# Optimization experiments

Hardware: AMD Instinct MI355X
Metric: run time of the kernel (lower is better)

## Reference

```python
import jax, jax.numpy as jnp
import numpy as np

NUM_HEADS = 16
D_MODEL = 1024
BATCH = 4
SEQ = 1024


def setup_inputs() -> dict:
    key = jax.random.key(0)
    k_x, k_m, k_wqkv, k_bqkv, k_wo, k_bo = jax.random.split(key, 6)
    d = D_MODEL
    scale = 1.0 / np.sqrt(d)
    return {
        "x": jax.random.normal(k_x, (BATCH, SEQ, d), dtype=jnp.float32),
        "mask": jax.random.randint(k_m, (BATCH, SEQ, SEQ), 0, 2, dtype=jnp.int32),
        "Wqkv": jax.random.normal(k_wqkv, (d, 3 * d), dtype=jnp.float32) * scale,
        "bqkv": jax.random.normal(k_bqkv, (3 * d,), dtype=jnp.float32) * 0.02,
        "Wo": jax.random.normal(k_wo, (d, d), dtype=jnp.float32) * scale,
        "bo": jax.random.normal(k_bo, (d,), dtype=jnp.float32) * 0.02,
    }


def reference(x, mask, Wqkv, bqkv, Wo, bo):
    B, S, D = x.shape
    H = NUM_HEADS
    hd = D // H
    # fused QKV projection: [B,S,3D] -> [B,S,H,3*hd] -> [B,H,S,3*hd]
    qkv = (x @ Wqkv + bqkv).reshape(B, S, H, 3 * hd).transpose(0, 2, 1, 3)
    q, k, v = jnp.split(qkv, 3, axis=-1)  # each [B,H,S,hd]
    # scores [B,H,S,S], scaled by sqrt(head_dim)
    scores = jnp.einsum("bhqd,bhkd->bhqk", q, k) / jnp.sqrt(jnp.float32(hd))
    scores = jnp.where(mask[:, None, :, :] == 0, jnp.float32(-1e20), scores)
    attn = jax.nn.softmax(scores, axis=-1)
    vals = jnp.einsum("bhqk,bhkd->bhqd", attn, v)  # [B,H,S,hd]
    vals = vals.transpose(0, 2, 1, 3).reshape(B, S, D)
    return vals @ Wo + bo
```

## Files before the change

### kernel.cpp

```cpp
#include <hip/hip_runtime.h>
#include <cstddef>
#include <cstdint>

#define BATCH 4
#define SEQ   1024
#define DM    1024
#define NH    16
#define HD    64
#define D3    3072
#define LOG2E 1.44269504088896340736f
#define QSCALE (0.125f * LOG2E)

typedef _Float16 f16x8 __attribute__((ext_vector_type(8)));
typedef _Float16 f16x4 __attribute__((ext_vector_type(4)));
typedef __fp16   h16x2 __attribute__((ext_vector_type(2)));
typedef float    f32x4 __attribute__((ext_vector_type(4)));

#define MFMA16(a, b, c) __builtin_amdgcn_mfma_f32_16x16x32_f16((a), (b), (c), 0, 0, 0)
#define GLD_LDS16(gp, lp) \
  __builtin_amdgcn_global_load_lds((const __attribute__((address_space(1))) unsigned int*)(gp), \
                                   (__attribute__((address_space(3))) unsigned int*)(lp), 16, 0, 0)
#if __has_builtin(__builtin_amdgcn_exp2f)
#define EXP2(x) __builtin_amdgcn_exp2f(x)
#else
#define EXP2(x) exp2f(x)
#endif

__global__ __launch_bounds__(256) void prep_all(const float* __restrict__ x,
                                                _Float16* __restrict__ x16,
                                                const int* __restrict__ mask,
                                                unsigned long long* __restrict__ mb,
                                                const float* __restrict__ W1,
                                                _Float16* __restrict__ WT1,
                                                const float* __restrict__ W2,
                                                _Float16* __restrict__ WT2) {
  __shared__ _Float16 T[64 * 72];
  const int tid = threadIdx.x;
  const int bx = blockIdx.x;
  if (bx < 1024) {
    const int tx = bx & 63, ty = bx >> 6;
    const bool first = tx < 48;
    const float* W = first ? W1 : W2;
    _Float16* WT = first ? WT1 : WT2;
    const int N = first ? D3 : DM;
    const int K = DM;
    const int c0 = (first ? tx : (tx - 48)) * 64;
    const int r0 = ty * 64;
#pragma unroll
    for (int it = 0; it < 4; ++it) {
      const int row = it * 16 + (tid >> 4);
      const int col4 = (tid & 15) * 4;
      float4 wv = *(const float4*)(W + (size_t)(r0 + row) * N + c0 + col4);
      T[(col4 + 0) * 72 + row] = (_Float16)wv.x;
      T[(col4 + 1) * 72 + row] = (_Float16)wv.y;
      T[(col4 + 2) * 72 + row] = (_Float16)wv.z;
      T[(col4 + 3) * 72 + row] = (_Float16)wv.w;
    }
    __syncthreads();
#pragma unroll
    for (int it = 0; it < 2; ++it) {
      const int g = it * 256 + tid;
      const int col = g >> 3, seg = g & 7;
      *(f16x8*)(WT + (size_t)(c0 + col) * K + r0 + seg * 8) =
          *(const f16x8*)(T + col * 72 + seg * 8);
    }
  } else if (bx < 3072) {
    const int i = (bx - 1024) * 256 + tid;
    float4 a = ((const float4*)x)[i * 2];
    float4 b = ((const float4*)x)[i * 2 + 1];
    f16x8 o;
    o[0] = (_Float16)a.x; o[1] = (_Float16)a.y; o[2] = (_Float16)a.z; o[3] = (_Float16)a.w;
    o[4] = (_Float16)b.x; o[5] = (_Float16)b.y; o[6] = (_Float16)b.z; o[7] = (_Float16)b.w;
    ((f16x8*)x16)[i] = o;
  } else {
    const size_t i = (size_t)(bx - 3072) * 256 + tid;
    const int m = mask[i];
    unsigned long long bits = __ballot(m != 0);
    if ((tid & 63) == 0) mb[i >> 6] = bits;
  }
}

template <typename OutT, bool QKV, int TN, int BK>
__global__ __launch_bounds__(256) void gemm_bt(const _Float16* __restrict__ A,
                                               const _Float16* __restrict__ BT,
                                               const float* __restrict__ bias,
                                               OutT* __restrict__ C,
                                               _Float16* __restrict__ vTp,
                                               int M, int N, int K) {
  constexpr int NT = TN / 32;
  constexpr int CH = BK / 8;
  __shared__ _Float16 As[128 * BK];
  __shared__ _Float16 Bs[TN * BK];
  const int tid = threadIdx.x;
  const int l15 = tid & 15;
  const int quad = (tid & 63) >> 4;
  const int w = tid >> 6;
  const int wm = w >> 1, wn = w & 1;
  const int rowbase = blockIdx.y * 128;
  const int colbase = blockIdx.x * TN;

  f32x4 acc[4][NT];
#pragma unroll
  for (int mt = 0; mt < 4; ++mt)
#pragma unroll
    for (int nt = 0; nt < NT; ++nt) acc[mt][nt] = (f32x4){0.f, 0.f, 0.f, 0.f};

  for (int k0 = 0; k0 < K; k0 += BK) {
    __syncthreads();
#pragma unroll
    for (int it = 0; it < 128 * CH / 256; ++it) {
      const int g = it * 256 + tid;
      const int r = g / CH, cs = (g & (CH - 1)) ^ (r & (CH - 1));
      GLD_LDS16(A + (size_t)(rowbase + r) * K + k0 + cs * 8, As + g * 8);
    }
#pragma unroll
    for (int it = 0; it < TN * CH / 256; ++it) {
      const int g = it * 256 + tid;
      const int r = g / CH, cs = (g & (CH - 1)) ^ (r & (CH - 1));
      GLD_LDS16(BT + (size_t)(colbase + r) * K + k0 + cs * 8, Bs + g * 8);
    }
    __syncthreads();
#pragma unroll
    for (int kh = 0; kh < BK / 32; ++kh) {
      f16x8 a[4], b[NT];
#pragma unroll
      for (int mt = 0; mt < 4; ++mt) {
        const int row = wm * 64 + mt * 16 + l15;
        a[mt] = *(const f16x8*)(As + row * BK +
                                (((kh * 4 + quad) ^ (row & (CH - 1))) << 3));
      }
#pragma unroll
      for (int nt = 0; nt < NT; ++nt) {
        const int row = wn * (TN / 2) + nt * 16 + l15;
        b[nt] = *(const f16x8*)(Bs + row * BK +
                                (((kh * 4 + quad) ^ (row & (CH - 1))) << 3));
      }
#pragma unroll
      for (int mt = 0; mt < 4; ++mt)
#pragma unroll
        for (int nt = 0; nt < NT; ++nt)
          acc[mt][nt] = MFMA16(a[mt], b[nt], acc[mt][nt]);
    }
  }

  float bv[NT];
#pragma unroll
  for (int nt = 0; nt < NT; ++nt) bv[nt] = bias[colbase + wn * (TN / 2) + nt * 16 + l15];
#pragma unroll
  for (int mt = 0; mt < 4; ++mt)
#pragma unroll
    for (int nt = 0; nt < NT; ++nt) {
      const int col = colbase + wn * (TN / 2) + nt * 16 + l15;
      if (QKV) {
        const int reg3 = (col >> 6) % 3;
        if (reg3 == 2) {
          const int hh = col / 192;
          const int d = col - hh * 192 - 128;
          const int row0 = rowbase + wm * 64 + mt * 16 + quad * 4;
          const int bb = row0 >> 10, s0 = row0 & 1023;
          f16x4 pk;
#pragma unroll
          for (int r = 0; r < 4; ++r) pk[r] = (_Float16)(acc[mt][nt][r] + bv[nt]);
          *(f16x4*)(vTp + ((size_t)((bb * NH + hh) * HD + d)) * SEQ + s0) = pk;
        } else {
          const float sc = (reg3 == 0) ? QSCALE : 1.f;
#pragma unroll
          for (int r = 0; r < 4; ++r) {
            const int row = rowbase + wm * 64 + mt * 16 + quad * 4 + r;
            C[(size_t)row * N + col] = (OutT)((acc[mt][nt][r] + bv[nt]) * sc);
          }
        }
      } else {
#pragma unroll
        for (int r = 0; r < 4; ++r) {
          const int row = rowbase + wm * 64 + mt * 16 + quad * 4 + r;
          C[(size_t)row * N + col] = (OutT)(acc[mt][nt][r] + bv[nt]);
        }
      }
    }
}

__global__ __launch_bounds__(256) void attn(const _Float16* __restrict__ qkv,
                                            const _Float16* __restrict__ vT,
                                            const unsigned long long* __restrict__ mb,
                                            _Float16* __restrict__ vals) {
  __shared__ _Float16 Ks[64 * 72];
  __shared__ _Float16 Vt[64 * 72];
  __shared__ _Float16 Ps[4][32 * 72];
  __shared__ __align__(8) _Float16 LUT[16][4];
  const int tid = threadIdx.x;
  const int l15 = tid & 15, quad = (tid & 63) >> 4, w = tid >> 6;
  const int i = blockIdx.x;
  const int bh = (i >> 6) * 8 + (i & 7);
  const int b = bh >> 4, h = bh & 15;
  const int q0 = ((i >> 3) & 7) << 7;

  if (tid < 16) {
    LUT[tid][0] = (tid & 1) ? (_Float16)1.f : (_Float16)0.f;
    LUT[tid][1] = (tid & 2) ? (_Float16)1.f : (_Float16)0.f;
    LUT[tid][2] = (tid & 4) ? (_Float16)1.f : (_Float16)0.f;
    LUT[tid][3] = (tid & 8) ? (_Float16)1.f : (_Float16)0.f;
  }

  const _Float16* qb = qkv + (size_t)b * SEQ * D3 + h * 192;
  f16x8 qf[2][2];
#pragma unroll
  for (int qn = 0; qn < 2; ++qn)
#pragma unroll
    for (int hf = 0; hf < 2; ++hf)
      qf[qn][hf] = *(const f16x8*)(qb + (size_t)(q0 + w * 32 + qn * 16 + l15) * D3 +
                                   hf * 32 + quad * 8);

  const _Float16* kg = qb + 64;
  const _Float16* vg = vT + (size_t)((b * NH + h) * HD) * SEQ;
  const int sr = tid >> 3, sseg = tid & 7;
  const int vd = tid >> 2, vs = tid & 3;
  const size_t mb0 = (size_t)(b * SEQ + q0 + w * 32 + l15) * 16;
  const size_t mb1 = (size_t)(b * SEQ + q0 + w * 32 + 16 + l15) * 16;

  f16x8 k0r = *(const f16x8*)(kg + (size_t)sr * D3 + sseg * 8);
  f16x8 k1r = *(const f16x8*)(kg + (size_t)(sr + 32) * D3 + sseg * 8);
  f16x8 v0r = *(const f16x8*)(vg + (size_t)vd * SEQ + vs * 8);
  f16x8 v1r = *(const f16x8*)(vg + (size_t)vd * SEQ + 32 + vs * 8);
  unsigned long long mr0 = mb[mb0], mr1 = mb[mb1];

  f32x4 lacc[2];
  f32x4 o_[2][4];
#pragma unroll
  for (int qn = 0; qn < 2; ++qn) {
    lacc[qn] = (f32x4){0.f, 0.f, 0.f, 0.f};
#pragma unroll
    for (int dt = 0; dt < 4; ++dt) o_[qn][dt] = (f32x4){0.f, 0.f, 0.f, 0.f};
  }
  f16x8 ones;
#pragma unroll
  for (int i2 = 0; i2 < 8; ++i2) ones[i2] = (_Float16)1.f;

  for (int kt = 0; kt < 16; ++kt) {
    if (kt) __syncthreads();
    *(f16x8*)(Ks + sr * 72 + sseg * 8) = k0r;
    *(f16x8*)(Ks + (sr + 32) * 72 + sseg * 8) = k1r;
    *(f16x8*)(Vt + vd * 72 + vs * 8) = v0r;
    *(f16x8*)(Vt + vd * 72 + 32 + vs * 8) = v1r;
    __syncthreads();
    const unsigned long long mc[2] = {mr0, mr1};
    if (kt < 15) {
      const int kn = (kt + 1) << 6;
      k0r = *(const f16x8*)(kg + (size_t)(kn + sr) * D3 + sseg * 8);
      k1r = *(const f16x8*)(kg + (size_t)(kn + sr + 32) * D3 + sseg * 8);
      v0r = *(const f16x8*)(vg + (size_t)vd * SEQ + kn + vs * 8);
      v1r = *(const f16x8*)(vg + (size_t)vd * SEQ + kn + 32 + vs * 8);
      mr0 = mb[mb0 + kt + 1];
      mr1 = mb[mb1 + kt + 1];
    }
    f32x4 st[4][2];
#pragma unroll
    for (int mt = 0; mt < 4; ++mt)
#pragma unroll
      for (int qn = 0; qn < 2; ++qn) st[mt][qn] = (f32x4){0.f, 0.f, 0.f, 0.f};
#pragma unroll
    for (int mt = 0; mt < 4; ++mt) {
      f16x8 ka0 = *(const f16x8*)(Ks + (mt * 16 + l15) * 72 + quad * 8);
      f16x8 ka1 = *(const f16x8*)(Ks + (mt * 16 + l15) * 72 + 32 + quad * 8);
#pragma unroll
      for (int qn = 0; qn < 2; ++qn) {
        st[mt][qn] = MFMA16(ka0, qf[qn][0], st[mt][qn]);
        st[mt][qn] = MFMA16(ka1, qf[qn][1], st[mt][qn]);
      }
    }
#pragma unroll
    for (int qn = 0; qn < 2; ++qn)
#pragma unroll
      for (int mt = 0; mt < 4; ++mt) {
        float e0 = EXP2(fminf(st[mt][qn][0], 15.f));
        float e1 = EXP2(fminf(st[mt][qn][1], 15.f));
        float e2 = EXP2(fminf(st[mt][qn][2], 15.f));
        float e3 = EXP2(fminf(st[mt][qn][3], 15.f));
        h16x2 lo = __builtin_amdgcn_cvt_pkrtz(e0, e1);
        h16x2 hi = __builtin_amdgcn_cvt_pkrtz(e2, e3);
        f16x4 pk;
        pk[0] = (_Float16)lo[0]; pk[1] = (_Float16)lo[1];
        pk[2] = (_Float16)hi[0]; pk[3] = (_Float16)hi[1];
        const unsigned nib = (unsigned)(mc[qn] >> (mt * 16 + quad * 4)) & 15u;
        pk *= *(const f16x4*)LUT[nib];
        *(f16x4*)(&Ps[w][(qn * 16 + l15) * 72 + mt * 16 + quad * 4]) = pk;
      }
    f16x8 pa[2][2];
#pragma unroll
    for (int qn = 0; qn < 2; ++qn) {
      pa[qn][0] = *(const f16x8*)(&Ps[w][(qn * 16 + l15) * 72 + quad * 8]);
      pa[qn][1] = *(const f16x8*)(&Ps[w][(qn * 16 + l15) * 72 + 32 + quad * 8]);
      lacc[qn] = MFMA16(pa[qn][0], ones, lacc[qn]);
      lacc[qn] = MFMA16(pa[qn][1], ones, lacc[qn]);
    }
#pragma unroll
    for (int dt = 0; dt < 4; ++dt) {
      f16x8 vb0 = *(const f16x8*)(Vt + (dt * 16 + l15) * 72 + quad * 8);
      f16x8 vb1 = *(const f16x8*)(Vt + (dt * 16 + l15) * 72 + 32 + quad * 8);
#pragma unroll
      for (int qn = 0; qn < 2; ++qn) {
        o_[qn][dt] = MFMA16(pa[qn][0], vb0, o_[qn][dt]);
        o_[qn][dt] = MFMA16(pa[qn][1], vb1, o_[qn][dt]);
      }
    }
  }
#pragma unroll
  for (int qn = 0; qn < 2; ++qn) {
    f32x4 inv;
#pragma unroll
    for (int r = 0; r < 4; ++r) inv[r] = 1.f / lacc[qn][r];
#pragma unroll
    for (int dt = 0; dt < 4; ++dt)
#pragma unroll
      for (int r = 0; r < 4; ++r)
        vals[(size_t)(b * SEQ + q0 + w * 32 + qn * 16 + quad * 4 + r) * DM +
             h * HD + dt * 16 + l15] = (_Float16)(o_[qn][dt][r] * inv[r]);
  }
}

extern "C" void kernel_launch(void* const* d_in, const int* in_sizes, int n_in,
                              void* d_out, int out_size, void* d_ws, size_t ws_size,
                              hipStream_t stream) {
  const float* x    = (const float*)d_in[0];
  const int*   mask = (const int*)  d_in[1];
  const float* Wqkv = (const float*)d_in[2];
  const float* bqkv = (const float*)d_in[3];
  const float* Wo   = (const float*)d_in[4];
  const float* bo   = (const float*)d_in[5];
  float* out = (float*)d_out;

  char* ws = (char*)d_ws;
  _Float16* qkv16  = (_Float16*)ws;                    ws += (size_t)BATCH*SEQ*D3*2;
  _Float16* vT16   = (_Float16*)ws;                    ws += (size_t)BATCH*DM*SEQ*2;
  _Float16* x16    = (_Float16*)ws;                    ws += (size_t)BATCH*SEQ*DM*2;
  _Float16* WqkvT  = (_Float16*)ws;                    ws += (size_t)DM*D3*2;
  _Float16* WoT    = (_Float16*)ws;                    ws += (size_t)DM*DM*2;
  _Float16* vals16 = (_Float16*)ws;                    ws += (size_t)BATCH*SEQ*DM*2;
  unsigned long long* mbits = (unsigned long long*)ws;

  prep_all<<<3072 + (BATCH*SEQ*SEQ)/256, 256, 0, stream>>>(
      x, x16, mask, mbits, Wqkv, WqkvT, Wo, WoT);

  gemm_bt<_Float16, true, 128, 64><<<dim3(D3/128, BATCH*SEQ/128), 256, 0, stream>>>(
      x16, WqkvT, bqkv, qkv16, vT16, BATCH*SEQ, D3, DM);
  attn<<<512, 256, 0, stream>>>(qkv16, vT16, mbits, vals16);
  gemm_bt<float, false, 64, 128><<<dim3(DM/64, (BATCH*SEQ)/128), 256, 0, stream>>>(
      vals16, WoT, bo, out, nullptr, BATCH*SEQ, DM, DM);
}
```

Before: 186.1 us.

## Double-buffer K/V tiles in attention and raise wave priority around MFMA

The attention kernel now keeps two LDS buffers for K and V. While the current tile is being computed, the next tile is written into the other buffer and global loads are issued two tiles ahead, which cuts the per-iteration barriers from two to one. s_setprio is also raised around the MFMA blocks so matrix work is favoured when waves contend. In exchange, K/V LDS use doubles and more registers stay live for the deeper prefetch, which may lower occupancy.

```diff
diff --git a/kernel.cpp b/kernel.cpp
--- a/kernel.cpp
+++ b/kernel.cpp
@@ -184,8 +184,8 @@
                                             const _Float16* __restrict__ vT,
                                             const unsigned long long* __restrict__ mb,
                                             _Float16* __restrict__ vals) {
-  __shared__ _Float16 Ks[64 * 72];
-  __shared__ _Float16 Vt[64 * 72];
+  __shared__ _Float16 Ks[2][64 * 72];
+  __shared__ _Float16 Vt[2][64 * 72];
   __shared__ _Float16 Ps[4][32 * 72];
   __shared__ __align__(8) _Float16 LUT[16][4];
   const int tid = threadIdx.x;
@@ -222,7 +222,16 @@
   f16x8 k1r = *(const f16x8*)(kg + (size_t)(sr + 32) * D3 + sseg * 8);
   f16x8 v0r = *(const f16x8*)(vg + (size_t)vd * SEQ + vs * 8);
   f16x8 v1r = *(const f16x8*)(vg + (size_t)vd * SEQ + 32 + vs * 8);
-  unsigned long long mr0 = mb[mb0], mr1 = mb[mb1];
+  unsigned long long mcur0 = mb[mb0], mcur1 = mb[mb1];
+  *(f16x8*)(Ks[0] + sr * 72 + sseg * 8) = k0r;
+  *(f16x8*)(Ks[0] + (sr + 32) * 72 + sseg * 8) = k1r;
+  *(f16x8*)(Vt[0] + vd * 72 + vs * 8) = v0r;
+  *(f16x8*)(Vt[0] + vd * 72 + 32 + vs * 8) = v1r;
+  k0r = *(const f16x8*)(kg + (size_t)(64 + sr) * D3 + sseg * 8);
+  k1r = *(const f16x8*)(kg + (size_t)(64 + sr + 32) * D3 + sseg * 8);
+  v0r = *(const f16x8*)(vg + (size_t)vd * SEQ + 64 + vs * 8);
+  v1r = *(const f16x8*)(vg + (size_t)vd * SEQ + 96 + vs * 8);
+  unsigned long long mnxt0 = mb[mb0 + 1], mnxt1 = mb[mb1 + 1];
 
   f32x4 lacc[2];
   f32x4 o_[2][4];
@@ -236,38 +245,48 @@
 #pragma unroll
   for (int i2 = 0; i2 < 8; ++i2) ones[i2] = (_Float16)1.f;
 
+  __syncthreads();
+
   for (int kt = 0; kt < 16; ++kt) {
-    if (kt) __syncthreads();
-    *(f16x8*)(Ks + sr * 72 + sseg * 8) = k0r;
-    *(f16x8*)(Ks + (sr + 32) * 72 + sseg * 8) = k1r;
-    *(f16x8*)(Vt + vd * 72 + vs * 8) = v0r;
-    *(f16x8*)(Vt + vd * 72 + 32 + vs * 8) = v1r;
-    __syncthreads();
-    const unsigned long long mc[2] = {mr0, mr1};
+    const int cur = kt & 1;
+    const _Float16* Kc = Ks[cur];
+    const _Float16* Vc = Vt[cur];
     if (kt < 15) {
-      const int kn = (kt + 1) << 6;
+      _Float16* Kn = Ks[cur ^ 1];
+      _Float16* Vn = Vt[cur ^ 1];
+      *(f16x8*)(Kn + sr * 72 + sseg * 8) = k0r;
+      *(f16x8*)(Kn + (sr + 32) * 72 + sseg * 8) = k1r;
+      *(f16x8*)(Vn + vd * 72 + vs * 8) = v0r;
+      *(f16x8*)(Vn + vd * 72 + 32 + vs * 8) = v1r;
+    }
+    const unsigned long long mc[2] = {mcur0, mcur1};
+    mcur0 = mnxt0; mcur1 = mnxt1;
+    if (kt < 14) {
+      const int kn = (kt + 2) << 6;
       k0r = *(const f16x8*)(kg + (size_t)(kn + sr) * D3 + sseg * 8);
       k1r = *(const f16x8*)(kg + (size_t)(kn + sr + 32) * D3 + sseg * 8);
       v0r = *(const f16x8*)(vg + (size_t)vd * SEQ + kn + vs * 8);
       v1r = *(const f16x8*)(vg + (size_t)vd * SEQ + kn + 32 + vs * 8);
-      mr0 = mb[mb0 + kt + 1];
-      mr1 = mb[mb1 + kt + 1];
+      mnxt0 = mb[mb0 + kt + 2];
+      mnxt1 = mb[mb1 + kt + 2];
     }
     f32x4 st[4][2];
 #pragma unroll
     for (int mt = 0; mt < 4; ++mt)
 #pragma unroll
       for (int qn = 0; qn < 2; ++qn) st[mt][qn] = (f32x4){0.f, 0.f, 0.f, 0.f};
+    __builtin_amdgcn_s_setprio(1);
 #pragma unroll
     for (int mt = 0; mt < 4; ++mt) {
-      f16x8 ka0 = *(const f16x8*)(Ks + (mt * 16 + l15) * 72 + quad * 8);
-      f16x8 ka1 = *(const f16x8*)(Ks + (mt * 16 + l15) * 72 + 32 + quad * 8);
+      f16x8 ka0 = *(const f16x8*)(Kc + (mt * 16 + l15) * 72 + quad * 8);
+      f16x8 ka1 = *(const f16x8*)(Kc + (mt * 16 + l15) * 72 + 32 + quad * 8);
 #pragma unroll
       for (int qn = 0; qn < 2; ++qn) {
         st[mt][qn] = MFMA16(ka0, qf[qn][0], st[mt][qn]);
         st[mt][qn] = MFMA16(ka1, qf[qn][1], st[mt][qn]);
       }
     }
+    __builtin_amdgcn_s_setprio(0);
 #pragma unroll
     for (int qn = 0; qn < 2; ++qn)
 #pragma unroll
@@ -293,16 +312,19 @@
       lacc[qn] = MFMA16(pa[qn][0], ones, lacc[qn]);
       lacc[qn] = MFMA16(pa[qn][1], ones, lacc[qn]);
     }
+    __builtin_amdgcn_s_setprio(1);
 #pragma unroll
     for (int dt = 0; dt < 4; ++dt) {
-      f16x8 vb0 = *(const f16x8*)(Vt + (dt * 16 + l15) * 72 + quad * 8);
-      f16x8 vb1 = *(const f16x8*)(Vt + (dt * 16 + l15) * 72 + 32 + quad * 8);
+      f16x8 vb0 = *(const f16x8*)(Vc + (dt * 16 + l15) * 72 + quad * 8);
+      f16x8 vb1 = *(const f16x8*)(Vc + (dt * 16 + l15) * 72 + 32 + quad * 8);
 #pragma unroll
       for (int qn = 0; qn < 2; ++qn) {
         o_[qn][dt] = MFMA16(pa[qn][0], vb0, o_[qn][dt]);
         o_[qn][dt] = MFMA16(pa[qn][1], vb1, o_[qn][dt]);
       }
     }
+    __builtin_amdgcn_s_setprio(0);
+    __syncthreads();
   }
 #pragma unroll
   for (int qn = 0; qn < 2; ++qn) {
```

New measurement: 179.2 us. 1.04x faster.
